# Kernel optimization log

Hardware: AMD Instinct MI355X
Metric: run time of the kernel (lower is better)

## Reference

```python
import jax, jax.numpy as jnp
import numpy as np

N = 4096   # number of observations
Q = 1024   # number of spatial locations (dist_matrix side)


def setup_inputs() -> dict:
    key = jax.random.key(0)
    k1, k2, k3, k4 = jax.random.split(key, 4)
    y_true = jax.random.normal(k1, (N, 1), dtype=jnp.float32)
    y_pred = jax.random.normal(k2, (N, 1), dtype=jnp.float32)
    Z_idx = jax.random.randint(k3, (N, 1), 0, Q).astype(jnp.int64)
    # symmetric distance matrix from random 2D coordinates
    coords = jax.random.uniform(k4, (Q, 2), dtype=jnp.float32) * 10.0
    diff = coords[:, None, :] - coords[None, :, :]
    dist_matrix = jnp.sqrt(jnp.sum(diff * diff, axis=-1) + 1e-12)
    sig2e = jnp.asarray(1.0, dtype=jnp.float32)
    sig2bs = jnp.ones((2,), dtype=jnp.float32)
    return {"y_true": y_true, "y_pred": y_pred, "Z_idx": Z_idx,
            "dist_matrix": dist_matrix, "sig2e": sig2e, "sig2bs": sig2bs}


def reference(y_true, y_pred, Z_idx, dist_matrix, sig2e, sig2bs):
    # NLL for the 'spatial' mixed-effects mode (custom_loss_lm).
    # V = sig2e*I + Z D Z^T with Z the one-hot indicator of Z_idx and
    # D[a,b] = sig2bs[0]*exp(-dist[a,b]/(2*sig2bs[1])).
    # Z D Z^T for one-hot Z is simply the row/col gather D[idx][:, idx],
    # which avoids materializing the dense N x Q indicator matrix.
    n = y_true.shape[0]
    idx = Z_idx[:, 0]
    D = sig2bs[0] * jnp.exp(-dist_matrix / (2.0 * sig2bs[1]))   # (Q, Q)
    V = sig2e * jnp.eye(n, dtype=jnp.float32) + D[idx][:, idx]  # (N, N)
    r = y_true - y_pred                                          # (N, 1)
    V_inv_r = jnp.linalg.solve(V, r)                             # (N, 1)
    quad = jnp.sum(r * V_inv_r)
    _, logdet = jnp.linalg.slogdet(V)
    log2pi = jnp.asarray(np.log(2.0 * np.pi), dtype=jnp.float32)
    total_loss = 0.5 * n * log2pi + 0.5 * logdet + 0.5 * quad
    return total_loss
```

## Files before the change

### kernel.cpp

```cpp
#include <hip/hip_runtime.h>
#include <math.h>

#define NN 4096
#define QQ 1024
#define LDA 1032
#define AF (1025 * 1032)

__global__ void k_stats(const float* __restrict__ yt, const float* __restrict__ yp,
                        const int* __restrict__ idx, float* __restrict__ s,
                        int* __restrict__ c, float* __restrict__ scal) {
    int i = blockIdx.x * 256 + threadIdx.x;
    float r = yt[i] - yp[i];
    int q = idx[i];
    atomicAdd(&s[q], r);
    atomicAdd(&c[q], 1);
    float v = r * r;
    for (int o = 32; o > 0; o >>= 1) v += __shfl_down(v, o, 64);
    __shared__ float red[4];
    int lane = threadIdx.x & 63, wid = threadIdx.x >> 6;
    if (lane == 0) red[wid] = v;
    __syncthreads();
    if (threadIdx.x == 0) atomicAdd(&scal[0], red[0] + red[1] + red[2] + red[3]);
}

__global__ void k_matvec(const float* __restrict__ dist, const float* __restrict__ s,
                         const int* __restrict__ c, float* __restrict__ t,
                         float* __restrict__ w, float* __restrict__ sqc,
                         float* __restrict__ scal, const float* __restrict__ sbs) {
    int i = blockIdx.x;
    float sb0 = sbs[0];
    float inv2 = 1.0f / (2.0f * sbs[1]);
    const float* dr = dist + (size_t)i * QQ;
    float acc = 0.f;
    for (int j = threadIdx.x; j < QQ; j += 256)
        acc += __expf(-dr[j] * inv2) * s[j];
    for (int o = 32; o > 0; o >>= 1) acc += __shfl_down(acc, o, 64);
    __shared__ float red[4];
    int lane = threadIdx.x & 63, wid = threadIdx.x >> 6;
    if (lane == 0) red[wid] = acc;
    __syncthreads();
    if (threadIdx.x == 0) {
        float tot = (red[0] + red[1] + red[2] + red[3]) * sb0;
        t[i] = tot;
        float sq = sqrtf((float)c[i]);
        sqc[i] = sq;
        w[i] = sq * tot;
        atomicAdd(&scal[1], s[i] * tot);
    }
}

__global__ void k_build(const float* __restrict__ dist, const float* __restrict__ sqc,
                        const float* __restrict__ w, float* __restrict__ A,
                        const float* __restrict__ se_p, const float* __restrict__ sbs) {
    int i = blockIdx.x;
    if (i == QQ) {
        for (int j = threadIdx.x; j < QQ; j += 256) A[(size_t)QQ * LDA + j] = w[j];
        return;
    }
    float sb0 = sbs[0];
    float inv2 = 1.0f / (2.0f * sbs[1]);
    float inv_se = 1.0f / se_p[0];
    float qi = sqc[i] * inv_se * sb0;
    const float* dr = dist + (size_t)i * QQ;
    float* ar = A + (size_t)i * LDA;
    for (int j = threadIdx.x; j < QQ; j += 256)
        ar[j] = ((i == j) ? 1.0f : 0.0f) + qi * sqc[j] * __expf(-dr[j] * inv2);
}

__device__ __forceinline__ void potrf64_run(float (&x)[16], int i, int q,
                                            float2 (&col2)[2][64]) {
#pragma unroll
    for (int qk = 0; qk < 4; ++qk) {
#pragma unroll
        for (int c2 = 0; c2 < 8; ++c2) {
            const int k = qk * 16 + 2 * c2;
            const int ck = 2 * c2;
            const int b = c2 & 1;
            if (q == qk) {
                float xk = x[ck];
                float d0 = __shfl(xk, k, 64);
                float rs0 = rsqrtf(d0);
                float l0 = (i == k) ? d0 * rs0 : xk * rs0;
                if (i >= k) x[ck] = l0;
                float lk1 = __shfl(l0, k + 1, 64);
                float x1v = fmaf(-l0, lk1, x[ck + 1]);
                float d1 = __shfl(x1v, k + 1, 64);
                float rs1 = rsqrtf(d1);
                float l1 = (i == k + 1) ? d1 * rs1 : x1v * rs1;
                if (i >= k + 1) x[ck + 1] = l1;
                col2[b][i] = make_float2(l0, l1);
            }
            __syncthreads();
            if (16 * q + 15 > k + 1 && i > k) {
                float2 lp = col2[b][i];
                const float4* cp = (const float4*)(&col2[b][16 * q]);
#pragma unroll
                for (int m2 = 0; m2 < 8; ++m2) {
                    float4 v = cp[m2];
                    if (16 * q + 2 * m2 > k + 1)
                        x[2 * m2] = fmaf(-lp.x, v.x, fmaf(-lp.y, v.y, x[2 * m2]));
                    if (16 * q + 2 * m2 + 1 > k + 1)
                        x[2 * m2 + 1] = fmaf(-lp.x, v.z, fmaf(-lp.y, v.w, x[2 * m2 + 1]));
                }
            }
        }
    }
}

__global__ __launch_bounds__(256) void k_potrf0(float* __restrict__ A) {
    __shared__ float2 col2[2][64];
    int tid = threadIdx.x, i = tid & 63, q = tid >> 6;
    float* row = A + (size_t)i * LDA + 16 * q;
    float x[16];
#pragma unroll
    for (int m4 = 0; m4 < 4; ++m4) {
        float4 v = ((const float4*)row)[m4];
        x[4 * m4] = v.x; x[4 * m4 + 1] = v.y; x[4 * m4 + 2] = v.z; x[4 * m4 + 3] = v.w;
    }
    potrf64_run(x, i, q, col2);
#pragma unroll
    for (int m4 = 0; m4 < 4; ++m4)
        ((float4*)row)[m4] = make_float4(x[4 * m4], x[4 * m4 + 1], x[4 * m4 + 2], x[4 * m4 + 3]);
}

template<int K, int M>
struct TAcc {
    static __device__ __forceinline__ void run(const float (&Lb)[64][65], const float (&x)[64],
                                               float& a0, float& a1) {
        if constexpr (M < K)     a0 = fmaf(-Lb[K][M], x[M], a0);
        if constexpr (M + 1 < K) a1 = fmaf(-Lb[K][M + 1], x[M + 1], a1);
        if constexpr (M + 2 < K) TAcc<K, M + 2>::run(Lb, x, a0, a1);
    }
};
template<int K>
struct TStep {
    static __device__ __forceinline__ void run(const float (&Lb)[64][65], const float (&dinv)[64],
                                               float (&x)[64]) {
        if constexpr (K < 64) {
            float a0 = x[K], a1 = 0.f;
            TAcc<K, 0>::run(Lb, x, a0, a1);
            x[K] = (a0 + a1) * dinv[K];
            TStep<K + 1>::run(Lb, dinv, x);
        }
    }
};

__global__ __launch_bounds__(64, 2) void k_trsm(float* __restrict__ A, int p) {
    __shared__ float Lb[64][65];
    __shared__ float dinv[64];
    int t = threadIdx.x;
    const float* db = A + (size_t)(p * 64) * (LDA + 1);
    for (int i = 0; i < 64; ++i) Lb[i][t] = db[(size_t)i * LDA + t];
    dinv[t] = 1.0f / Lb[t][t];
    __syncthreads();
    int r = (p + 1) * 64 + blockIdx.x * 64 + t;
    if (r <= QQ) {
        float* ar = A + (size_t)r * LDA + p * 64;
        float x[64];
#pragma unroll
        for (int jj = 0; jj < 16; ++jj) {
            float4 v = ((const float4*)ar)[jj];
            x[4 * jj] = v.x; x[4 * jj + 1] = v.y; x[4 * jj + 2] = v.z; x[4 * jj + 3] = v.w;
        }
        TStep<0>::run(Lb, dinv, x);
#pragma unroll
        for (int jj = 0; jj < 16; ++jj)
            ((float4*)ar)[jj] = make_float4(x[4 * jj], x[4 * jj + 1], x[4 * jj + 2], x[4 * jj + 3]);
    }
}

__global__ __launch_bounds__(256) void k_syrkpotrf(float* __restrict__ A, int p) {
    int t0 = (p + 1) * 64;
    int r0 = t0 + blockIdx.y * 64;
    int c0 = t0 + blockIdx.x * 64;
    if (c0 > r0) return;
    bool dfuse = (blockIdx.x == 0 && blockIdx.y == 0);
    __shared__ __align__(16) float PrRaw[64 * 68];
    __shared__ __align__(16) float PcRaw[64 * 68];
    __shared__ float2 col2[2][64];
    int tid = threadIdx.x;
    int tx = tid & 15, ty = tid >> 4;
    int pc0 = p * 64;
    for (int idx2 = tid; idx2 < 1024; idx2 += 256) {
        int rr = idx2 >> 4, c4 = idx2 & 15;
        int gr = r0 + rr;
        float4 v = make_float4(0.f, 0.f, 0.f, 0.f);
        if (gr <= QQ) v = *(const float4*)(A + (size_t)gr * LDA + pc0 + 4 * c4);
        *(float4*)(PrRaw + rr * 68 + 4 * c4) = v;
        if (!dfuse) {
            float4 u = *(const float4*)(A + (size_t)(c0 + rr) * LDA + pc0 + 4 * c4);
            *(float4*)(PcRaw + rr * 68 + 4 * c4) = u;
        }
    }
    __syncthreads();
    const float* PB = dfuse ? PrRaw : PcRaw;
    float acc[4][4];
#pragma unroll
    for (int ii = 0; ii < 4; ++ii)
#pragma unroll
        for (int jj = 0; jj < 4; ++jj) acc[ii][jj] = 0.f;
    float4 ar[4], br[4];
#pragma unroll 4
    for (int k4 = 0; k4 < 16; ++k4) {
#pragma unroll
        for (int ii = 0; ii < 4; ++ii)
            ar[ii] = *(const float4*)(PrRaw + (ty + 16 * ii) * 68 + 4 * k4);
#pragma unroll
        for (int jj = 0; jj < 4; ++jj)
            br[jj] = *(const float4*)(PB + (tx + 16 * jj) * 68 + 4 * k4);
#pragma unroll
        for (int ii = 0; ii < 4; ++ii)
#pragma unroll
            for (int jj = 0; jj < 4; ++jj) {
                acc[ii][jj] = fmaf(ar[ii].x, br[jj].x, acc[ii][jj]);
                acc[ii][jj] = fmaf(ar[ii].y, br[jj].y, acc[ii][jj]);
                acc[ii][jj] = fmaf(ar[ii].z, br[jj].z, acc[ii][jj]);
                acc[ii][jj] = fmaf(ar[ii].w, br[jj].w, acc[ii][jj]);
            }
    }
    if (!dfuse) {
#pragma unroll
        for (int ii = 0; ii < 4; ++ii) {
            int rr = r0 + ty + 16 * ii;
            if (rr <= QQ) {
#pragma unroll
                for (int jj = 0; jj < 4; ++jj) {
                    float* pa = A + (size_t)rr * LDA + c0 + tx + 16 * jj;
                    *pa -= acc[ii][jj];
                }
            }
        }
    } else {
#pragma unroll
        for (int ii = 0; ii < 4; ++ii) {
            int lr = ty + 16 * ii;
#pragma unroll
            for (int jj = 0; jj < 4; ++jj) {
                int lc = tx + 16 * jj;
                float old = A[(size_t)(r0 + lr) * LDA + c0 + lc];
                PcRaw[lr * 65 + lc] = old - acc[ii][jj];
            }
        }
        __syncthreads();
        int i = tid & 63, q = tid >> 6;
        float x[16];
#pragma unroll
        for (int m = 0; m < 16; ++m) x[m] = PcRaw[i * 65 + 16 * q + m];
        potrf64_run(x, i, q, col2);
        float* row = A + (size_t)(r0 + i) * LDA + c0 + 16 * q;
#pragma unroll
        for (int m4 = 0; m4 < 4; ++m4)
            ((float4*)row)[m4] = make_float4(x[4 * m4], x[4 * m4 + 1],
                                             x[4 * m4 + 2], x[4 * m4 + 3]);
    }
}

__global__ void k_final(const float* __restrict__ A, const float* __restrict__ scal,
                        const float* __restrict__ se_p, float* __restrict__ out) {
    int i = threadIdx.x;
    float v1 = 2.0f * __logf(A[(size_t)i * LDA + i]);
    float yv = A[(size_t)QQ * LDA + i];
    float v2 = yv * yv;
    for (int o = 32; o > 0; o >>= 1) {
        v1 += __shfl_down(v1, o, 64);
        v2 += __shfl_down(v2, o, 64);
    }
    __shared__ float r1[16], r2[16];
    int lane = i & 63, wid = i >> 6;
    if (lane == 0) { r1[wid] = v1; r2[wid] = v2; }
    __syncthreads();
    if (i == 0) {
        float ld = 0.f, yy = 0.f;
        for (int k = 0; k < 16; ++k) { ld += r1[k]; yy += r2[k]; }
        float se = se_p[0], inv = 1.0f / se;
        float rr = scal[0], st = scal[1];
        float quad = rr * inv - inv * inv * (st - inv * yy);
        float logdetV = (float)NN * __logf(se) + ld;
        out[0] = 0.5f * (float)NN * 1.8378770664093453f + 0.5f * logdetV + 0.5f * quad;
    }
}

extern "C" void kernel_launch(void* const* d_in, const int* in_sizes, int n_in,
                              void* d_out, int out_size, void* d_ws, size_t ws_size,
                              hipStream_t stream) {
    const float* yt   = (const float*)d_in[0];
    const float* yp   = (const float*)d_in[1];
    const int*   idx  = (const int*)d_in[2];
    const float* dist = (const float*)d_in[3];
    const float* se   = (const float*)d_in[4];
    const float* sbs  = (const float*)d_in[5];
    float* out = (float*)d_out;

    float* W    = (float*)d_ws;
    float* A    = W;
    int*   c    = (int*)(W + AF);
    float* s    = W + AF + 1024;
    float* scal = W + AF + 2048;
    float* t    = scal + 2;
    float* w    = t + 1024;
    float* sqc  = w + 1024;

    hipMemsetAsync(c, 0, (1024 + 1024 + 2) * sizeof(float), stream);

    k_stats<<<dim3(NN / 256), dim3(256), 0, stream>>>(yt, yp, idx, s, c, scal);
    k_matvec<<<dim3(QQ), dim3(256), 0, stream>>>(dist, s, c, t, w, sqc, scal, sbs);
    k_build<<<dim3(QQ + 1), dim3(256), 0, stream>>>(dist, sqc, w, A, se, sbs);

    k_potrf0<<<dim3(1), dim3(256), 0, stream>>>(A);
    for (int p = 0; p < 15; ++p) {
        int rows = (QQ + 1) - (p + 1) * 64;
        k_trsm<<<dim3((rows + 63) / 64), dim3(64), 0, stream>>>(A, p);
        int ncol = (QQ - (p + 1) * 64) / 64;
        int nr = (rows + 63) / 64;
        k_syrkpotrf<<<dim3(ncol, nr), dim3(256), 0, stream>>>(A, p);
    }
    k_trsm<<<dim3(1), dim3(64), 0, stream>>>(A, 15);
    k_final<<<dim3(1), dim3(1024), 0, stream>>>(A, scal, se, out);
}
```

Before: 688.4 us.

## Replace per-panel Cholesky launches with persistent dataflow kernel using atomic work queue

Replaces the 32 separate potrf/trsm/syrk launches and the final reduction kernel with a single persistent kernel. Blocks pull tiles from an atomic counter in dependency order and spin on acquire/release flags for panel, trsm and update readiness. This removes launch overhead and the global barriers between panel steps, so trailing updates can overlap the next panel. In exchange it adds spin-wait latency and relies on work-ordering to avoid deadlock, and the trsm now uses 256-thread blocks with only 64 threads active.

```diff
diff --git a/kernel.cpp b/kernel.cpp
--- a/kernel.cpp
+++ b/kernel.cpp
@@ -107,22 +107,6 @@
     }
 }
 
-__global__ __launch_bounds__(256) void k_potrf0(float* __restrict__ A) {
-    __shared__ float2 col2[2][64];
-    int tid = threadIdx.x, i = tid & 63, q = tid >> 6;
-    float* row = A + (size_t)i * LDA + 16 * q;
-    float x[16];
-#pragma unroll
-    for (int m4 = 0; m4 < 4; ++m4) {
-        float4 v = ((const float4*)row)[m4];
-        x[4 * m4] = v.x; x[4 * m4 + 1] = v.y; x[4 * m4 + 2] = v.z; x[4 * m4 + 3] = v.w;
-    }
-    potrf64_run(x, i, q, col2);
-#pragma unroll
-    for (int m4 = 0; m4 < 4; ++m4)
-        ((float4*)row)[m4] = make_float4(x[4 * m4], x[4 * m4 + 1], x[4 * m4 + 2], x[4 * m4 + 3]);
-}
-
 template<int K, int M>
 struct TAcc {
     static __device__ __forceinline__ void run(const float (&Lb)[64][65], const float (&x)[64],
@@ -145,138 +129,223 @@
     }
 };
 
-__global__ __launch_bounds__(64, 2) void k_trsm(float* __restrict__ A, int p) {
-    __shared__ float Lb[64][65];
-    __shared__ float dinv[64];
-    int t = threadIdx.x;
-    const float* db = A + (size_t)(p * 64) * (LDA + 1);
-    for (int i = 0; i < 64; ++i) Lb[i][t] = db[(size_t)i * LDA + t];
-    dinv[t] = 1.0f / Lb[t][t];
-    __syncthreads();
-    int r = (p + 1) * 64 + blockIdx.x * 64 + t;
-    if (r <= QQ) {
-        float* ar = A + (size_t)r * LDA + p * 64;
-        float x[64];
-#pragma unroll
-        for (int jj = 0; jj < 16; ++jj) {
-            float4 v = ((const float4*)ar)[jj];
-            x[4 * jj] = v.x; x[4 * jj + 1] = v.y; x[4 * jj + 2] = v.z; x[4 * jj + 3] = v.w;
-        }
-        TStep<0>::run(Lb, dinv, x);
-#pragma unroll
-        for (int jj = 0; jj < 16; ++jj)
-            ((float4*)ar)[jj] = make_float4(x[4 * jj], x[4 * jj + 1], x[4 * jj + 2], x[4 * jj + 3]);
-    }
-}
-
-__global__ __launch_bounds__(256) void k_syrkpotrf(float* __restrict__ A, int p) {
-    int t0 = (p + 1) * 64;
-    int r0 = t0 + blockIdx.y * 64;
-    int c0 = t0 + blockIdx.x * 64;
-    if (c0 > r0) return;
-    bool dfuse = (blockIdx.x == 0 && blockIdx.y == 0);
-    __shared__ __align__(16) float PrRaw[64 * 68];
-    __shared__ __align__(16) float PcRaw[64 * 68];
+__device__ __forceinline__ int ld_acq(int* p) {
+    return __hip_atomic_load(p, __ATOMIC_ACQUIRE, __HIP_MEMORY_SCOPE_AGENT);
+}
+__device__ __forceinline__ void st_rel(int* p, int v) {
+    __hip_atomic_store(p, v, __ATOMIC_RELEASE, __HIP_MEMORY_SCOPE_AGENT);
+}
+__device__ __forceinline__ void spin_eq(int* p, int v) {
+    while (ld_acq(p) < v) __builtin_amdgcn_s_sleep(2);
+}
+
+__global__ __launch_bounds__(256, 2) void k_chol(float* __restrict__ A, int* __restrict__ cq,
+                                                 const float* __restrict__ scal,
+                                                 const float* __restrict__ se_p,
+                                                 float* __restrict__ out) {
+    __shared__ __align__(16) float ShA[64 * 68];
+    __shared__ __align__(16) float ShB[64 * 68];
     __shared__ float2 col2[2][64];
+    __shared__ int item[4];
+    __shared__ float fred[2][4];
     int tid = threadIdx.x;
-    int tx = tid & 15, ty = tid >> 4;
-    int pc0 = p * 64;
-    for (int idx2 = tid; idx2 < 1024; idx2 += 256) {
-        int rr = idx2 >> 4, c4 = idx2 & 15;
-        int gr = r0 + rr;
-        float4 v = make_float4(0.f, 0.f, 0.f, 0.f);
-        if (gr <= QQ) v = *(const float4*)(A + (size_t)gr * LDA + pc0 + 4 * c4);
-        *(float4*)(PrRaw + rr * 68 + 4 * c4) = v;
-        if (!dfuse) {
-            float4 u = *(const float4*)(A + (size_t)(c0 + rr) * LDA + pc0 + 4 * c4);
-            *(float4*)(PcRaw + rr * 68 + 4 * c4) = u;
-        }
-    }
-    __syncthreads();
-    const float* PB = dfuse ? PrRaw : PcRaw;
-    float acc[4][4];
-#pragma unroll
-    for (int ii = 0; ii < 4; ++ii)
-#pragma unroll
-        for (int jj = 0; jj < 4; ++jj) acc[ii][jj] = 0.f;
-    float4 ar[4], br[4];
-#pragma unroll 4
-    for (int k4 = 0; k4 < 16; ++k4) {
-#pragma unroll
-        for (int ii = 0; ii < 4; ++ii)
-            ar[ii] = *(const float4*)(PrRaw + (ty + 16 * ii) * 68 + 4 * k4);
-#pragma unroll
-        for (int jj = 0; jj < 4; ++jj)
-            br[jj] = *(const float4*)(PB + (tx + 16 * jj) * 68 + 4 * k4);
-#pragma unroll
-        for (int ii = 0; ii < 4; ++ii)
-#pragma unroll
-            for (int jj = 0; jj < 4; ++jj) {
-                acc[ii][jj] = fmaf(ar[ii].x, br[jj].x, acc[ii][jj]);
-                acc[ii][jj] = fmaf(ar[ii].y, br[jj].y, acc[ii][jj]);
-                acc[ii][jj] = fmaf(ar[ii].z, br[jj].z, acc[ii][jj]);
-                acc[ii][jj] = fmaf(ar[ii].w, br[jj].w, acc[ii][jj]);
-            }
-    }
-    if (!dfuse) {
-#pragma unroll
-        for (int ii = 0; ii < 4; ++ii) {
-            int rr = r0 + ty + 16 * ii;
-            if (rr <= QQ) {
-#pragma unroll
-                for (int jj = 0; jj < 4; ++jj) {
-                    float* pa = A + (size_t)rr * LDA + c0 + tx + 16 * jj;
-                    *pa -= acc[ii][jj];
-                }
-            }
-        }
-    } else {
-#pragma unroll
-        for (int ii = 0; ii < 4; ++ii) {
-            int lr = ty + 16 * ii;
-#pragma unroll
-            for (int jj = 0; jj < 4; ++jj) {
-                int lc = tx + 16 * jj;
-                float old = A[(size_t)(r0 + lr) * LDA + c0 + lc];
-                PcRaw[lr * 65 + lc] = old - acc[ii][jj];
-            }
+    int* qc = cq;
+    int* pf = cq + 1;
+    int* td = cq + 17;
+    int* uc = cq + 17 + 272;
+
+    for (;;) {
+        if (tid == 0) {
+            int idx = atomicAdd(qc, 1);
+            int ty = 4, pp = 0, ii = 0, jj = 0;
+            if (idx == 0) ty = 0;
+            else if (idx == 937) ty = 3;
+            else if (idx < 937) {
+                int r = idx - 1;
+                for (int p = 0; p < 16; ++p) {
+                    int n1 = 16 - p;
+                    if (r < n1) { ty = 1; pp = p; ii = p + 1 + r; break; }
+                    r -= n1;
+                    int ng = (16 - p) * (17 - p) / 2 - 1;
+                    if (r < ng) {
+                        ty = 2; pp = p;
+                        for (int j = p + 1; j <= 15; ++j) {
+                            int cnt = 17 - j;
+                            if (r < cnt) { jj = j; ii = j + r; break; }
+                            r -= cnt;
+                        }
+                        break;
+                    }
+                    r -= ng;
+                }
+            }
+            item[0] = ty; item[1] = pp; item[2] = ii; item[3] = jj;
         }
         __syncthreads();
-        int i = tid & 63, q = tid >> 6;
-        float x[16];
-#pragma unroll
-        for (int m = 0; m < 16; ++m) x[m] = PcRaw[i * 65 + 16 * q + m];
-        potrf64_run(x, i, q, col2);
-        float* row = A + (size_t)(r0 + i) * LDA + c0 + 16 * q;
-#pragma unroll
-        for (int m4 = 0; m4 < 4; ++m4)
-            ((float4*)row)[m4] = make_float4(x[4 * m4], x[4 * m4 + 1],
-                                             x[4 * m4 + 2], x[4 * m4 + 3]);
-    }
-}
-
-__global__ void k_final(const float* __restrict__ A, const float* __restrict__ scal,
-                        const float* __restrict__ se_p, float* __restrict__ out) {
-    int i = threadIdx.x;
-    float v1 = 2.0f * __logf(A[(size_t)i * LDA + i]);
-    float yv = A[(size_t)QQ * LDA + i];
-    float v2 = yv * yv;
-    for (int o = 32; o > 0; o >>= 1) {
-        v1 += __shfl_down(v1, o, 64);
-        v2 += __shfl_down(v2, o, 64);
-    }
-    __shared__ float r1[16], r2[16];
-    int lane = i & 63, wid = i >> 6;
-    if (lane == 0) { r1[wid] = v1; r2[wid] = v2; }
-    __syncthreads();
-    if (i == 0) {
-        float ld = 0.f, yy = 0.f;
-        for (int k = 0; k < 16; ++k) { ld += r1[k]; yy += r2[k]; }
-        float se = se_p[0], inv = 1.0f / se;
-        float rr = scal[0], st = scal[1];
-        float quad = rr * inv - inv * inv * (st - inv * yy);
-        float logdetV = (float)NN * __logf(se) + ld;
-        out[0] = 0.5f * (float)NN * 1.8378770664093453f + 0.5f * logdetV + 0.5f * quad;
+        int ty = item[0], p = item[1], ci = item[2], cj = item[3];
+        __syncthreads();
+        if (ty == 4) return;
+
+        if (ty == 0) {
+            int i = tid & 63, q = tid >> 6;
+            float* row = A + (size_t)i * LDA + 16 * q;
+            float x[16];
+#pragma unroll
+            for (int m4 = 0; m4 < 4; ++m4) {
+                float4 v = ((const float4*)row)[m4];
+                x[4 * m4] = v.x; x[4 * m4 + 1] = v.y; x[4 * m4 + 2] = v.z; x[4 * m4 + 3] = v.w;
+            }
+            potrf64_run(x, i, q, col2);
+#pragma unroll
+            for (int m4 = 0; m4 < 4; ++m4)
+                ((float4*)row)[m4] = make_float4(x[4 * m4], x[4 * m4 + 1], x[4 * m4 + 2], x[4 * m4 + 3]);
+            __syncthreads();
+            if (tid == 0) st_rel(&pf[0], 1);
+
+        } else if (ty == 1) {
+            spin_eq(&pf[p], 1);
+            spin_eq(&uc[ci * 16 + p], p);
+            float (*Lb)[65] = (float(*)[65])ShA;
+            float* dinv = ShB;
+            const float* db = A + (size_t)(p * 64) * LDA + p * 64;
+            for (int idx2 = tid; idx2 < 4096; idx2 += 256) {
+                int r = idx2 >> 6, cc = idx2 & 63;
+                Lb[r][cc] = db[(size_t)r * LDA + cc];
+            }
+            __syncthreads();
+            if (tid < 64) dinv[tid] = 1.0f / Lb[tid][tid];
+            __syncthreads();
+            if (tid < 64) {
+                int r = ci * 64 + tid;
+                if (r <= QQ) {
+                    float* ar = A + (size_t)r * LDA + p * 64;
+                    float x[64];
+#pragma unroll
+                    for (int jj4 = 0; jj4 < 16; ++jj4) {
+                        float4 v = ((const float4*)ar)[jj4];
+                        x[4 * jj4] = v.x; x[4 * jj4 + 1] = v.y; x[4 * jj4 + 2] = v.z; x[4 * jj4 + 3] = v.w;
+                    }
+                    TStep<0>::run(*(const float(*)[64][65])Lb, *(const float(*)[64])dinv, x);
+#pragma unroll
+                    for (int jj4 = 0; jj4 < 16; ++jj4)
+                        ((float4*)ar)[jj4] = make_float4(x[4 * jj4], x[4 * jj4 + 1], x[4 * jj4 + 2], x[4 * jj4 + 3]);
+                }
+            }
+            __syncthreads();
+            if (tid == 0) st_rel(&td[ci * 16 + p], 1);
+
+        } else if (ty == 2) {
+            bool diag = (ci == cj);
+            bool dfuse = diag && (cj == p + 1);
+            spin_eq(&td[ci * 16 + p], 1);
+            if (!diag) spin_eq(&td[cj * 16 + p], 1);
+            spin_eq(&uc[ci * 16 + cj], p);
+            int r0 = ci * 64, c0 = cj * 64, pc0 = p * 64;
+            for (int idx2 = tid; idx2 < 1024; idx2 += 256) {
+                int rr = idx2 >> 4, c4 = idx2 & 15;
+                int gr = r0 + rr;
+                float4 v = make_float4(0.f, 0.f, 0.f, 0.f);
+                if (gr <= QQ) v = *(const float4*)(A + (size_t)gr * LDA + pc0 + 4 * c4);
+                *(float4*)(ShA + rr * 68 + 4 * c4) = v;
+                if (!diag) {
+                    float4 u = *(const float4*)(A + (size_t)(c0 + rr) * LDA + pc0 + 4 * c4);
+                    *(float4*)(ShB + rr * 68 + 4 * c4) = u;
+                }
+            }
+            __syncthreads();
+            const float* PB = diag ? ShA : ShB;
+            int tx = tid & 15, ty2 = tid >> 4;
+            float acc[4][4];
+#pragma unroll
+            for (int a = 0; a < 4; ++a)
+#pragma unroll
+                for (int b = 0; b < 4; ++b) acc[a][b] = 0.f;
+            float4 arg[4], brg[4];
+#pragma unroll 4
+            for (int k4 = 0; k4 < 16; ++k4) {
+#pragma unroll
+                for (int a = 0; a < 4; ++a)
+                    arg[a] = *(const float4*)(ShA + (ty2 + 16 * a) * 68 + 4 * k4);
+#pragma unroll
+                for (int b = 0; b < 4; ++b)
+                    brg[b] = *(const float4*)(PB + (tx + 16 * b) * 68 + 4 * k4);
+#pragma unroll
+                for (int a = 0; a < 4; ++a)
+#pragma unroll
+                    for (int b = 0; b < 4; ++b) {
+                        acc[a][b] = fmaf(arg[a].x, brg[b].x, acc[a][b]);
+                        acc[a][b] = fmaf(arg[a].y, brg[b].y, acc[a][b]);
+                        acc[a][b] = fmaf(arg[a].z, brg[b].z, acc[a][b]);
+                        acc[a][b] = fmaf(arg[a].w, brg[b].w, acc[a][b]);
+                    }
+            }
+            if (!dfuse) {
+#pragma unroll
+                for (int a = 0; a < 4; ++a) {
+                    int rr = r0 + ty2 + 16 * a;
+                    if (rr <= QQ) {
+#pragma unroll
+                        for (int b = 0; b < 4; ++b)
+                            A[(size_t)rr * LDA + c0 + tx + 16 * b] -= acc[a][b];
+                    }
+                }
+                __syncthreads();
+                if (tid == 0) st_rel(&uc[ci * 16 + cj], p + 1);
+            } else {
+#pragma unroll
+                for (int a = 0; a < 4; ++a) {
+                    int lr = ty2 + 16 * a;
+#pragma unroll
+                    for (int b = 0; b < 4; ++b) {
+                        int lc = tx + 16 * b;
+                        float old = A[(size_t)(r0 + lr) * LDA + c0 + lc];
+                        ShB[lr * 65 + lc] = old - acc[a][b];
+                    }
+                }
+                __syncthreads();
+                int i = tid & 63, q = tid >> 6;
+                float x[16];
+#pragma unroll
+                for (int m = 0; m < 16; ++m) x[m] = ShB[i * 65 + 16 * q + m];
+                potrf64_run(x, i, q, col2);
+                float* row = A + (size_t)(r0 + i) * LDA + c0 + 16 * q;
+#pragma unroll
+                for (int m4 = 0; m4 < 4; ++m4)
+                    ((float4*)row)[m4] = make_float4(x[4 * m4], x[4 * m4 + 1],
+                                                     x[4 * m4 + 2], x[4 * m4 + 3]);
+                __syncthreads();
+                if (tid == 0) { st_rel(&uc[ci * 16 + cj], p + 1); st_rel(&pf[p + 1], 1); }
+            }
+
+        } else {
+            spin_eq(&pf[15], 1);
+            spin_eq(&td[16 * 16 + 15], 1);
+            float v1 = 0.f, v2 = 0.f;
+#pragma unroll
+            for (int m = 0; m < 4; ++m) {
+                int i = tid * 4 + m;
+                v1 += 2.0f * __logf(A[(size_t)i * LDA + i]);
+                float yv = A[(size_t)QQ * LDA + i];
+                v2 += yv * yv;
+            }
+            for (int o = 32; o > 0; o >>= 1) {
+                v1 += __shfl_down(v1, o, 64);
+                v2 += __shfl_down(v2, o, 64);
+            }
+            int lane = tid & 63, wid = tid >> 6;
+            if (lane == 0) { fred[0][wid] = v1; fred[1][wid] = v2; }
+            __syncthreads();
+            if (tid == 0) {
+                float ld = fred[0][0] + fred[0][1] + fred[0][2] + fred[0][3];
+                float yy = fred[1][0] + fred[1][1] + fred[1][2] + fred[1][3];
+                float se = se_p[0], inv = 1.0f / se;
+                float rr = scal[0], st = scal[1];
+                float quad = rr * inv - inv * inv * (st - inv * yy);
+                float logdetV = (float)NN * __logf(se) + ld;
+                out[0] = 0.5f * (float)NN * 1.8378770664093453f + 0.5f * logdetV + 0.5f * quad;
+            }
+            __syncthreads();
+        }
     }
 }
 
@@ -296,24 +365,15 @@
     int*   c    = (int*)(W + AF);
     float* s    = W + AF + 1024;
     float* scal = W + AF + 2048;
-    float* t    = scal + 2;
+    int*   cq   = (int*)(W + AF + 2056);
+    float* t    = (float*)(cq + 561);
     float* w    = t + 1024;
     float* sqc  = w + 1024;
 
-    hipMemsetAsync(c, 0, (1024 + 1024 + 2) * sizeof(float), stream);
+    hipMemsetAsync(c, 0, (1024 + 1024 + 8 + 561) * sizeof(float), stream);
 
     k_stats<<<dim3(NN / 256), dim3(256), 0, stream>>>(yt, yp, idx, s, c, scal);
     k_matvec<<<dim3(QQ), dim3(256), 0, stream>>>(dist, s, c, t, w, sqc, scal, sbs);
     k_build<<<dim3(QQ + 1), dim3(256), 0, stream>>>(dist, sqc, w, A, se, sbs);
-
-    k_potrf0<<<dim3(1), dim3(256), 0, stream>>>(A);
-    for (int p = 0; p < 15; ++p) {
-        int rows = (QQ + 1) - (p + 1) * 64;
-        k_trsm<<<dim3((rows + 63) / 64), dim3(64), 0, stream>>>(A, p);
-        int ncol = (QQ - (p + 1) * 64) / 64;
-        int nr = (rows + 63) / 64;
-        k_syrkpotrf<<<dim3(ncol, nr), dim3(256), 0, stream>>>(A, p);
-    }
-    k_trsm<<<dim3(1), dim3(64), 0, stream>>>(A, 15);
-    k_final<<<dim3(1), dim3(1024), 0, stream>>>(A, scal, se, out);
-}
+    k_chol<<<dim3(160), dim3(256), 0, stream>>>(A, cq, scal, se, out);
+}
```

Measured after the change: 1.720 ms. 2.5x slower.
